# Performance work log

Hardware: AMD Instinct MI355X
Metric: run time of the kernel (lower is better)

Reference implementation:

```python
import jax, jax.numpy as jnp
import numpy as np

EPS = float(jnp.finfo(jnp.float32).eps)


def _mlp(x, W1, b1, W2, b2, W3, b3):
    h = jax.nn.relu(x @ W1 + b1)
    h = jax.nn.relu(h @ W2 + b2)
    return h @ W3 + b3


def setup_inputs() -> dict:
    B, D_A, D_B, K, H = 131072, 16, 16, 32, 256
    key = jax.random.key(0)
    ks = jax.random.split(key, 13)
    def lin(k, fi, fo):
        return jax.random.normal(k, (fi, fo), jnp.float32) * (fi ** -0.5)
    inp = {
        "x": jax.random.uniform(ks[0], (B, D_A + D_B), jnp.float32),
        "hW1": lin(ks[1], D_A, H), "hb1": jnp.zeros((H,), jnp.float32),
        "hW2": lin(ks[2], H, H),   "hb2": jnp.zeros((H,), jnp.float32),
        "hW3": lin(ks[3], H, D_B * (K + 1)), "hb3": jnp.zeros((D_B * (K + 1),), jnp.float32),
        "wW1": lin(ks[4], D_A, H), "wb1": jnp.zeros((H,), jnp.float32),
        "wW2": lin(ks[5], H, H),   "wb2": jnp.zeros((H,), jnp.float32),
        "wW3": lin(ks[6], H, D_B * K), "wb3": jnp.zeros((D_B * K,), jnp.float32),
        "A_dims": jnp.arange(0, 32, 2, dtype=jnp.int32),
        "B_dims": jnp.arange(1, 32, 2, dtype=jnp.int32),
    }
    return inp


def reference(x, hW1, hb1, hW2, hb2, hW3, hb3, wW1, wb1, wW2, wb2, wW3, wb3, A_dims, B_dims):
    B = x.shape[0]
    D_B = B_dims.shape[0]
    K = wW3.shape[1] // D_B
    x_A = x[:, A_dims]               # (B, D_A)
    x_B = x[:, B_dims]               # (B, D_B)

    raw_h = _mlp(x_A, hW1, hb1, hW2, hb2, hW3, hb3).reshape(B, D_B, K + 1)
    heights = jax.nn.softplus(raw_h) + EPS
    raw_w = _mlp(x_A, wW1, wb1, wW2, wb2, wW3, wb3).reshape(B, D_B, K)
    widths = jax.nn.softmax(raw_w, axis=-1)
    zeros = jnp.zeros((B, D_B, 1), x.dtype)
    bins = jnp.concatenate([zeros, jnp.cumsum(widths, axis=-1)], axis=-1)  # (B, D_B, K+1)

    # preprocess_params_2: normalise PDF heights and bin areas
    bin_widths = bins[:, :, 1:] - bins[:, :, :-1]
    bin_areas = 0.5 * (heights[:, :, :-1] + heights[:, :, 1:]) * bin_widths  # (B, D_B, K)
    total_area = bin_areas.sum(axis=-1, keepdims=True)
    v = heights / total_area
    bin_areas = bin_areas / total_area

    # bin search
    i = jnp.sum(x_B[..., None] >= bins, axis=-1) - 1
    i = jnp.clip(i, 0, K - 1)                                  # (B, D_B)
    iu = i[..., None]

    x_left = jnp.take_along_axis(bins, iu, axis=2)[..., 0]
    x_right = jnp.take_along_axis(bins, iu + 1, axis=2)[..., 0]
    w_b = x_right - x_left
    v_left = jnp.take_along_axis(v, iu, axis=2)[..., 0]
    v_right = jnp.take_along_axis(v, iu + 1, axis=2)[..., 0]
    w_v = v_right - v_left

    alpha = (x_B - x_left) / (w_b + EPS)
    # cumulative area up to left edge of bin i: exclusive prefix sum then gather
    c_edges = jnp.concatenate([zeros, jnp.cumsum(bin_areas, axis=-1)], axis=-1)
    c_left = jnp.take_along_axis(c_edges, iu, axis=2)[..., 0]

    y_B = c_left + 0.5 * alpha ** 2 * w_v * w_b + alpha * v_left * w_b
    y = x.at[:, B_dims].set(y_B)
    return y
```

## Files before the change

kernel.cpp:

```cpp
#include <hip/hip_runtime.h>
#include <cmath>

typedef short short8 __attribute__((ext_vector_type(8)));
typedef short short4v __attribute__((ext_vector_type(4)));
typedef float f32x16 __attribute__((ext_vector_type(16)));

#define EPSF 1.1920929e-07f

#define LDS_A2W 0
#define LDS_A2H 33792
#define LDS_A1W 67584
#define LDS_A1H 101376
#define LDS_XA  135168
#define LDS_EW  67584
#define LDS_HH  104448
#define LDS_TOTAL 141312

#define OFF1H 0
#define OFF1W 4096
#define OFF2H 8192
#define OFF2W 73728
#define OFF3H 139264
#define OFF3W 278528

__device__ __forceinline__ unsigned short f2bf(float f) {
  union { float f; unsigned u; } v; v.f = f;
  return (unsigned short)((v.u + 0x8000u) >> 16);
}
__device__ __forceinline__ float bf2f(unsigned short h) {
  union { unsigned u; float f; } v; v.u = ((unsigned)h) << 16; return v.f;
}

__global__ void pack_weights(const float* __restrict__ hW1, const float* __restrict__ wW1,
                             const float* __restrict__ hW2, const float* __restrict__ wW2,
                             const float* __restrict__ hW3, const float* __restrict__ wW3,
                             unsigned short* __restrict__ out) {
  int tile = blockIdx.x, l = threadIdx.x;
  const float* src; unsigned short* dst; int NT, N, K, base;
  if (tile < 8)        { src = hW1; dst = out + OFF1H; NT = 8;  N = 256; K = 16;  base = tile; }
  else if (tile < 16)  { src = wW1; dst = out + OFF1W; NT = 8;  N = 256; K = 16;  base = tile - 8; }
  else if (tile < 144) { src = hW2; dst = out + OFF2H; NT = 8;  N = 256; K = 256; base = tile - 16; }
  else if (tile < 272) { src = wW2; dst = out + OFF2W; NT = 8;  N = 256; K = 256; base = tile - 144; }
  else if (tile < 544) { src = hW3; dst = out + OFF3H; NT = 17; N = 528; K = 256; base = tile - 272; }
  else                 { src = wW3; dst = out + OFF3W; NT = 16; N = 512; K = 256; base = tile - 544; }
  int nt = base % NT, kt = base / NT, KTT = K / 16;
  int n = nt * 32 + (l & 31);
  int k0 = kt * 16 + (l >> 5) * 8;
  short8 v;
  #pragma unroll
  for (int e = 0; e < 8; e++) {
    float f = (n < N && (k0 + e) < K) ? src[(k0 + e) * N + n] : 0.f;
    v[e] = (short)f2bf(f);
  }
  int idx = nt * KTT + kt;
  *(short8*)(dst + (idx * 64 + l) * 8) = v;
}

struct Acc2 { f32x16 a0, a1; };

template <int KT>
__device__ __forceinline__ Acc2 gemm_tile2(const unsigned short* __restrict__ A, int apitch,
                                           const unsigned short* __restrict__ pB, int ct,
                                           float init) {
  int l = threadIdx.x & 63;
  Acc2 r;
  #pragma unroll
  for (int i = 0; i < 16; i++) { r.a0[i] = init; r.a1[i] = init; }
  const unsigned short* aptr0 = A + (l & 31) * apitch + (l >> 5) * 8;
  const unsigned short* aptr1 = aptr0 + 32 * apitch;
  const unsigned short* bptr = pB + (ct * KT * 64 + l) * 8;
  #pragma unroll
  for (int kt = 0; kt < KT; kt++) {
    short8 b = *(const short8*)(bptr + kt * 512);
    short8 a0 = *(const short8*)(aptr0 + kt * 16);
    short8 a1 = *(const short8*)(aptr1 + kt * 16);
    r.a0 = __builtin_amdgcn_mfma_f32_32x32x16_bf16(a0, b, r.a0, 0, 0, 0);
    r.a1 = __builtin_amdgcn_mfma_f32_32x32x16_bf16(a1, b, r.a1, 0, 0, 0);
  }
  return r;
}

__device__ __forceinline__ void epi_relu2(char* lds, int oOff, Acc2 a, int ct) {
  int l = threadIdx.x & 63;
  int col = ct * 32 + (l & 31);
  unsigned short* o = (unsigned short*)(lds + oOff) + col + 4 * (l >> 5) * 264;
  #pragma unroll
  for (int r = 0; r < 16; r++) {
    int row = (r & 3) + 8 * (r >> 2);
    o[row * 264] = f2bf(fmaxf(a.a0[r], 0.f));
    o[(row + 32) * 264] = f2bf(fmaxf(a.a1[r], 0.f));
  }
}

__global__ __launch_bounds__(1024, 4) void fused_kernel(
    const float* __restrict__ x,
    const float* __restrict__ hb1, const float* __restrict__ hb2, const float* __restrict__ hb3,
    const float* __restrict__ wb1, const float* __restrict__ wb2, const float* __restrict__ wb3,
    const unsigned short* __restrict__ pw,
    float* __restrict__ y) {
  extern __shared__ char lds[];
  const int t = threadIdx.x;
  const int w = t >> 6, l = t & 63;
  const int r0 = blockIdx.x * 64;

  if (t < 512) {
    int row = t >> 3, c4 = t & 7;
    float4 v = *(const float4*)(x + (r0 + row) * 32 + c4 * 4);
    y[(r0 + row) * 32 + c4 * 4] = v.x;
    y[(r0 + row) * 32 + c4 * 4 + 2] = v.z;
    unsigned short* xa = (unsigned short*)(lds + LDS_XA) + row * 16 + c4 * 2;
    xa[0] = f2bf(v.x); xa[1] = f2bf(v.z);
  }
  __syncthreads();

  const unsigned short* XA  = (const unsigned short*)(lds + LDS_XA);
  const unsigned short* A1W = (const unsigned short*)(lds + LDS_A1W);
  const unsigned short* A1H = (const unsigned short*)(lds + LDS_A1H);
  const unsigned short* A2W = (const unsigned short*)(lds + LDS_A2W);
  const unsigned short* A2H = (const unsigned short*)(lds + LDS_A2H);
  const int ct8 = w & 7;
  const int col8 = ct8 * 32 + (l & 31);

  if (w < 8) { epi_relu2(lds, LDS_A1W, gemm_tile2<1>(XA, 16, pw + OFF1W, ct8, wb1[col8]), ct8); }
  else       { epi_relu2(lds, LDS_A1H, gemm_tile2<1>(XA, 16, pw + OFF1H, ct8, hb1[col8]), ct8); }
  __syncthreads();
  if (w < 8) { epi_relu2(lds, LDS_A2W, gemm_tile2<16>(A1W, 264, pw + OFF2W, ct8, wb2[col8]), ct8); }
  else       { epi_relu2(lds, LDS_A2H, gemm_tile2<16>(A1H, 264, pw + OFF2H, ct8, hb2[col8]), ct8); }
  __syncthreads();

  #pragma unroll 1
  for (int H = 0; H < 2; H++) {
    for (int u = w; u < 17; u += 16) {
      if (u < 8) {
        int ctg = H * 8 + u;
        Acc2 a = gemm_tile2<16>(A2W, 264, pw + OFF3W, ctg, wb3[ctg * 32 + (l & 31)]);
        unsigned short* o = (unsigned short*)(lds + LDS_EW) + (ctg & 7) * 36 + (l & 31)
                            + 4 * (l >> 5) * 288;
        #pragma unroll
        for (int r = 0; r < 16; r++) {
          int row = (r & 3) + 8 * (r >> 2);
          o[row * 288] = f2bf(__expf(a.a0[r]));
          o[(row + 32) * 288] = f2bf(__expf(a.a1[r]));
        }
      } else {
        int ctg = (u - 8) + 8 * H;
        int c = ctg * 32 + (l & 31);
        float bv = (c < 528) ? hb3[c] : 0.f;
        Acc2 a = gemm_tile2<16>(A2H, 264, pw + OFF3H, ctg, bv);
        if (c >= 264 * H && c < 264 * (H + 1)) {
          unsigned d = ((unsigned)c * 993u) >> 15;
          int j = c - 33 * (int)d;
          unsigned short* o = (unsigned short*)(lds + LDS_HH) + ((int)d & 7) * 36 + j
                              + 4 * (l >> 5) * 288;
          #pragma unroll
          for (int r = 0; r < 16; r++) {
            int row = (r & 3) + 8 * (r >> 2);
            float v0 = a.a0[r];
            o[row * 288] = f2bf(fmaxf(v0, 0.f) + __logf(1.f + __expf(-fabsf(v0))) + EPSF);
            float v1 = a.a1[r];
            o[(row + 32) * 288] = f2bf(fmaxf(v1, 0.f) + __logf(1.f + __expf(-fabsf(v1))) + EPSF);
          }
        }
      }
    }
    __syncthreads();

    {
      int p = t >> 1, half = t & 1;
      int row = p >> 3, dl = p & 7, dg = H * 8 + dl;
      const unsigned short* EWb = (const unsigned short*)(lds + LDS_EW) + row * 288 + dl * 36;
      const unsigned short* HHb = (const unsigned short*)(lds + LDS_HH) + row * 288 + dl * 36;
      const unsigned short* EWp = EWb + half * 16;
      const unsigned short* HHp = HHb + half * 16;
      float e[16], hh[17];
      #pragma unroll
      for (int i = 0; i < 4; i++) {
        short4v ev = *(const short4v*)(EWp + i * 4);
        short4v hv = *(const short4v*)(HHp + i * 4);
        #pragma unroll
        for (int jj = 0; jj < 4; jj++) {
          e[i * 4 + jj] = bf2f((unsigned short)ev[jj]);
          hh[i * 4 + jj] = bf2f((unsigned short)hv[jj]);
        }
      }
      hh[16] = bf2f(HHp[16]);
      float se = 0.f;
      #pragma unroll
      for (int k = 0; k < 16; k++) se += e[k];
      float so = __shfl_xor(se, 1);
      float s = se + so;
      float xbv = x[(r0 + row) * 32 + 2 * dg + 1];
      float xbs = xbv * s;
      float bl0 = half ? so : 0.f;
      int fnd = (xbs >= bl0) ? 1 : 0;
      float bl = bl0, cl2 = 0.f, sxl = bl0, scl2 = 0.f;
      int ki = 0;
      #pragma unroll
      for (int k = 0; k < 16; k++) {
        bool c = (xbs >= bl);
        ki   = c ? k   : ki;
        sxl  = c ? bl  : sxl;
        scl2 = c ? cl2 : scl2;
        cl2 += (hh[k] + hh[k + 1]) * e[k];
        bl  += e[k];
      }
      float cl2o = __shfl_xor(cl2, 1);
      float S2 = cl2 + cl2o;
      if (half) scl2 += cl2o;
      int   o_ki   = __shfl_xor(ki, 1);
      float o_sxl  = __shfl_xor(sxl, 1);
      float o_scl2 = __shfl_xor(scl2, 1);
      int   o_fnd  = __shfl_xor(fnd, 1);
      bool other = half ? (fnd == 0) : (o_fnd != 0);
      int   gki   = other ? o_ki   : ki;
      int   ghalf = other ? (half ^ 1) : half;
      float gsxl  = other ? o_sxl  : sxl;
      float gscl2 = other ? o_scl2 : scl2;
      int go = ghalf * 16 + gki;
      float sew = bf2f(EWb[go]);
      float shl = bf2f(HHb[go]);
      float shr = bf2f(HHb[go + 1]);
      float alpha = (xbs - gsxl) / (sew + EPSF);
      float yv = (gscl2 + (alpha * alpha * (shr - shl) + 2.f * alpha * shl) * sew) / S2;
      if (!half) y[(r0 + row) * 32 + 2 * dg + 1] = yv;
    }
    __syncthreads();
  }
}

extern "C" void kernel_launch(void* const* d_in, const int* in_sizes, int n_in,
                              void* d_out, int out_size, void* d_ws, size_t ws_size,
                              hipStream_t stream) {
  const float* x   = (const float*)d_in[0];
  const float* hW1 = (const float*)d_in[1];
  const float* hb1 = (const float*)d_in[2];
  const float* hW2 = (const float*)d_in[3];
  const float* hb2 = (const float*)d_in[4];
  const float* hW3 = (const float*)d_in[5];
  const float* hb3 = (const float*)d_in[6];
  const float* wW1 = (const float*)d_in[7];
  const float* wb1 = (const float*)d_in[8];
  const float* wW2 = (const float*)d_in[9];
  const float* wb2 = (const float*)d_in[10];
  const float* wW3 = (const float*)d_in[11];
  const float* wb3 = (const float*)d_in[12];
  unsigned short* pw = (unsigned short*)d_ws;

  pack_weights<<<800, 64, 0, stream>>>(hW1, wW1, hW2, wW2, hW3, wW3, pw);

  hipFuncSetAttribute((const void*)fused_kernel,
                      hipFuncAttributeMaxDynamicSharedMemorySize, LDS_TOTAL);
  fused_kernel<<<2048, 1024, LDS_TOTAL, stream>>>(
      x, hb1, hb2, hb3, wb1, wb2, wb3, pw, (float*)d_out);
}
```

Before: 190.5 us.

## Prefetch next-layer weight fragments into registers during MFMA loops and unroll H phases

Restructures the fused MLP+spline kernel so each wave prefetches its layer-2 and layer-3 weight fragments from global memory into registers while the previous layer's MFMA loop runs, unrolls the two H phases explicitly, and preloads the x values used by the spline step. __syncthreads is replaced with an lgkmcnt wait plus s_barrier, and launch bounds drop from 4 to 1 block per CU minimum. The aim is to hide global weight-load latency behind matrix math. In exchange register pressure rises sharply (16-32 short8 fragments held live), and the new barrier only waits on LDS/scalar counters.

```diff
diff --git a/kernel.cpp b/kernel.cpp
--- a/kernel.cpp
+++ b/kernel.cpp
@@ -22,6 +22,11 @@
 #define OFF2W 73728
 #define OFF3H 139264
 #define OFF3W 278528
+
+#define LGKM_BARRIER() do { \
+  asm volatile("s_waitcnt lgkmcnt(0)" ::: "memory"); \
+  __builtin_amdgcn_s_barrier(); \
+} while (0)
 
 __device__ __forceinline__ unsigned short f2bf(float f) {
   union { float f; unsigned u; } v; v.f = f;
@@ -58,29 +63,16 @@
 
 struct Acc2 { f32x16 a0, a1; };
 
-template <int KT>
-__device__ __forceinline__ Acc2 gemm_tile2(const unsigned short* __restrict__ A, int apitch,
-                                           const unsigned short* __restrict__ pB, int ct,
-                                           float init) {
-  int l = threadIdx.x & 63;
+#define MFMA(A, B, C) __builtin_amdgcn_mfma_f32_32x32x16_bf16((A), (B), (C), 0, 0, 0)
+
+__device__ __forceinline__ Acc2 acc_init(float v) {
   Acc2 r;
   #pragma unroll
-  for (int i = 0; i < 16; i++) { r.a0[i] = init; r.a1[i] = init; }
-  const unsigned short* aptr0 = A + (l & 31) * apitch + (l >> 5) * 8;
-  const unsigned short* aptr1 = aptr0 + 32 * apitch;
-  const unsigned short* bptr = pB + (ct * KT * 64 + l) * 8;
-  #pragma unroll
-  for (int kt = 0; kt < KT; kt++) {
-    short8 b = *(const short8*)(bptr + kt * 512);
-    short8 a0 = *(const short8*)(aptr0 + kt * 16);
-    short8 a1 = *(const short8*)(aptr1 + kt * 16);
-    r.a0 = __builtin_amdgcn_mfma_f32_32x32x16_bf16(a0, b, r.a0, 0, 0, 0);
-    r.a1 = __builtin_amdgcn_mfma_f32_32x32x16_bf16(a1, b, r.a1, 0, 0, 0);
-  }
+  for (int i = 0; i < 16; i++) { r.a0[i] = v; r.a1[i] = v; }
   return r;
 }
 
-__device__ __forceinline__ void epi_relu2(char* lds, int oOff, Acc2 a, int ct) {
+__device__ __forceinline__ void epi_relu2(char* lds, int oOff, const Acc2& a, int ct) {
   int l = threadIdx.x & 63;
   int col = ct * 32 + (l & 31);
   unsigned short* o = (unsigned short*)(lds + oOff) + col + 4 * (l >> 5) * 264;
@@ -92,7 +84,97 @@
   }
 }
 
-__global__ __launch_bounds__(1024, 4) void fused_kernel(
+__device__ __forceinline__ void g3_epi(char* lds, const Acc2& a, int ctg, int H, bool wnet) {
+  int l = threadIdx.x & 63;
+  if (wnet) {
+    unsigned short* o = (unsigned short*)(lds + LDS_EW) + (ctg & 7) * 36 + (l & 31)
+                        + 4 * (l >> 5) * 288;
+    #pragma unroll
+    for (int r = 0; r < 16; r++) {
+      int row = (r & 3) + 8 * (r >> 2);
+      o[row * 288] = f2bf(__expf(a.a0[r]));
+      o[(row + 32) * 288] = f2bf(__expf(a.a1[r]));
+    }
+  } else {
+    int c = ctg * 32 + (l & 31);
+    if (c >= 264 * H && c < 264 * (H + 1)) {
+      unsigned d = ((unsigned)c * 993u) >> 15;
+      int j = c - 33 * (int)d;
+      unsigned short* o = (unsigned short*)(lds + LDS_HH) + ((int)d & 7) * 36 + j
+                          + 4 * (l >> 5) * 288;
+      #pragma unroll
+      for (int r = 0; r < 16; r++) {
+        int row = (r & 3) + 8 * (r >> 2);
+        float v0 = a.a0[r];
+        o[row * 288] = f2bf(fmaxf(v0, 0.f) + __logf(1.f + __expf(-fabsf(v0))) + EPSF);
+        float v1 = a.a1[r];
+        o[(row + 32) * 288] = f2bf(fmaxf(v1, 0.f) + __logf(1.f + __expf(-fabsf(v1))) + EPSF);
+      }
+    }
+  }
+}
+
+__device__ __forceinline__ void spline_phase(char* lds, int t, int H, float xbv,
+                                             float* __restrict__ y, int r0) {
+  int p = t >> 1, half = t & 1;
+  int row = p >> 3, dl = p & 7, dg = H * 8 + dl;
+  const unsigned short* EWb = (const unsigned short*)(lds + LDS_EW) + row * 288 + dl * 36;
+  const unsigned short* HHb = (const unsigned short*)(lds + LDS_HH) + row * 288 + dl * 36;
+  const unsigned short* EWp = EWb + half * 16;
+  const unsigned short* HHp = HHb + half * 16;
+  float e[16], hh[17];
+  #pragma unroll
+  for (int i = 0; i < 4; i++) {
+    short4v ev = *(const short4v*)(EWp + i * 4);
+    short4v hv = *(const short4v*)(HHp + i * 4);
+    #pragma unroll
+    for (int jj = 0; jj < 4; jj++) {
+      e[i * 4 + jj] = bf2f((unsigned short)ev[jj]);
+      hh[i * 4 + jj] = bf2f((unsigned short)hv[jj]);
+    }
+  }
+  hh[16] = bf2f(HHp[16]);
+  float se = 0.f;
+  #pragma unroll
+  for (int k = 0; k < 16; k++) se += e[k];
+  float so = __shfl_xor(se, 1);
+  float s = se + so;
+  float xbs = xbv * s;
+  float bl0 = half ? so : 0.f;
+  int fnd = (xbs >= bl0) ? 1 : 0;
+  float bl = bl0, cl2 = 0.f, sxl = bl0, scl2 = 0.f;
+  int ki = 0;
+  #pragma unroll
+  for (int k = 0; k < 16; k++) {
+    bool c = (xbs >= bl);
+    ki   = c ? k   : ki;
+    sxl  = c ? bl  : sxl;
+    scl2 = c ? cl2 : scl2;
+    cl2 += (hh[k] + hh[k + 1]) * e[k];
+    bl  += e[k];
+  }
+  float cl2o = __shfl_xor(cl2, 1);
+  float S2 = cl2 + cl2o;
+  if (half) scl2 += cl2o;
+  int   o_ki   = __shfl_xor(ki, 1);
+  float o_sxl  = __shfl_xor(sxl, 1);
+  float o_scl2 = __shfl_xor(scl2, 1);
+  int   o_fnd  = __shfl_xor(fnd, 1);
+  bool other = half ? (fnd == 0) : (o_fnd != 0);
+  int   gki   = other ? o_ki   : ki;
+  int   ghalf = other ? (half ^ 1) : half;
+  float gsxl  = other ? o_sxl  : sxl;
+  float gscl2 = other ? o_scl2 : scl2;
+  int go = ghalf * 16 + gki;
+  float sew = bf2f(EWb[go]);
+  float shl = bf2f(HHb[go]);
+  float shr = bf2f(HHb[go + 1]);
+  float alpha = (xbs - gsxl) / (sew + EPSF);
+  float yv = (gscl2 + (alpha * alpha * (shr - shl) + 2.f * alpha * shl) * sew) / S2;
+  if (!half) y[(r0 + row) * 32 + 2 * dg + 1] = yv;
+}
+
+__global__ __launch_bounds__(1024, 1) void fused_kernel(
     const float* __restrict__ x,
     const float* __restrict__ hb1, const float* __restrict__ hb2, const float* __restrict__ hb3,
     const float* __restrict__ wb1, const float* __restrict__ wb2, const float* __restrict__ wb3,
@@ -102,130 +184,138 @@
   const int t = threadIdx.x;
   const int w = t >> 6, l = t & 63;
   const int r0 = blockIdx.x * 64;
+  const bool wnet = (w < 8);
+  const int ct8 = w & 7;
+
+  float4 xv;
+  int xrow = t >> 3, xc4 = t & 7;
+  if (t < 512) xv = *(const float4*)(x + (r0 + xrow) * 32 + xc4 * 4);
+  int sp_p = t >> 1;
+  int sp_row = sp_p >> 3, sp_dl = sp_p & 7;
+  float xs0 = x[(r0 + sp_row) * 32 + 2 * sp_dl + 1];
+  float xs1 = x[(r0 + sp_row) * 32 + 2 * (8 + sp_dl) + 1];
+
+  const unsigned short* bL1 = pw + (wnet ? OFF1W : OFF1H) + (ct8 * 64 + l) * 8;
+  const unsigned short* bL2 = pw + (wnet ? OFF2W : OFF2H) + (ct8 * 16 * 64 + l) * 8;
+  short8 fL1 = *(const short8*)bL1;
+  short8 fL2[16];
+  #pragma unroll
+  for (int kt = 0; kt < 16; kt++) fL2[kt] = *(const short8*)(bL2 + kt * 512);
 
   if (t < 512) {
-    int row = t >> 3, c4 = t & 7;
-    float4 v = *(const float4*)(x + (r0 + row) * 32 + c4 * 4);
-    y[(r0 + row) * 32 + c4 * 4] = v.x;
-    y[(r0 + row) * 32 + c4 * 4 + 2] = v.z;
-    unsigned short* xa = (unsigned short*)(lds + LDS_XA) + row * 16 + c4 * 2;
-    xa[0] = f2bf(v.x); xa[1] = f2bf(v.z);
-  }
-  __syncthreads();
+    y[(r0 + xrow) * 32 + xc4 * 4] = xv.x;
+    y[(r0 + xrow) * 32 + xc4 * 4 + 2] = xv.z;
+    unsigned short* xa = (unsigned short*)(lds + LDS_XA) + xrow * 16 + xc4 * 2;
+    xa[0] = f2bf(xv.x); xa[1] = f2bf(xv.z);
+  }
+  LGKM_BARRIER();
 
   const unsigned short* XA  = (const unsigned short*)(lds + LDS_XA);
-  const unsigned short* A1W = (const unsigned short*)(lds + LDS_A1W);
-  const unsigned short* A1H = (const unsigned short*)(lds + LDS_A1H);
-  const unsigned short* A2W = (const unsigned short*)(lds + LDS_A2W);
-  const unsigned short* A2H = (const unsigned short*)(lds + LDS_A2H);
-  const int ct8 = w & 7;
   const int col8 = ct8 * 32 + (l & 31);
 
-  if (w < 8) { epi_relu2(lds, LDS_A1W, gemm_tile2<1>(XA, 16, pw + OFF1W, ct8, wb1[col8]), ct8); }
-  else       { epi_relu2(lds, LDS_A1H, gemm_tile2<1>(XA, 16, pw + OFF1H, ct8, hb1[col8]), ct8); }
-  __syncthreads();
-  if (w < 8) { epi_relu2(lds, LDS_A2W, gemm_tile2<16>(A1W, 264, pw + OFF2W, ct8, wb2[col8]), ct8); }
-  else       { epi_relu2(lds, LDS_A2H, gemm_tile2<16>(A1H, 264, pw + OFF2H, ct8, hb2[col8]), ct8); }
-  __syncthreads();
-
-  #pragma unroll 1
-  for (int H = 0; H < 2; H++) {
-    for (int u = w; u < 17; u += 16) {
-      if (u < 8) {
-        int ctg = H * 8 + u;
-        Acc2 a = gemm_tile2<16>(A2W, 264, pw + OFF3W, ctg, wb3[ctg * 32 + (l & 31)]);
-        unsigned short* o = (unsigned short*)(lds + LDS_EW) + (ctg & 7) * 36 + (l & 31)
-                            + 4 * (l >> 5) * 288;
-        #pragma unroll
-        for (int r = 0; r < 16; r++) {
-          int row = (r & 3) + 8 * (r >> 2);
-          o[row * 288] = f2bf(__expf(a.a0[r]));
-          o[(row + 32) * 288] = f2bf(__expf(a.a1[r]));
-        }
-      } else {
-        int ctg = (u - 8) + 8 * H;
-        int c = ctg * 32 + (l & 31);
-        float bv = (c < 528) ? hb3[c] : 0.f;
-        Acc2 a = gemm_tile2<16>(A2H, 264, pw + OFF3H, ctg, bv);
-        if (c >= 264 * H && c < 264 * (H + 1)) {
-          unsigned d = ((unsigned)c * 993u) >> 15;
-          int j = c - 33 * (int)d;
-          unsigned short* o = (unsigned short*)(lds + LDS_HH) + ((int)d & 7) * 36 + j
-                              + 4 * (l >> 5) * 288;
-          #pragma unroll
-          for (int r = 0; r < 16; r++) {
-            int row = (r & 3) + 8 * (r >> 2);
-            float v0 = a.a0[r];
-            o[row * 288] = f2bf(fmaxf(v0, 0.f) + __logf(1.f + __expf(-fabsf(v0))) + EPSF);
-            float v1 = a.a1[r];
-            o[(row + 32) * 288] = f2bf(fmaxf(v1, 0.f) + __logf(1.f + __expf(-fabsf(v1))) + EPSF);
-          }
-        }
-      }
-    }
-    __syncthreads();
-
-    {
-      int p = t >> 1, half = t & 1;
-      int row = p >> 3, dl = p & 7, dg = H * 8 + dl;
-      const unsigned short* EWb = (const unsigned short*)(lds + LDS_EW) + row * 288 + dl * 36;
-      const unsigned short* HHb = (const unsigned short*)(lds + LDS_HH) + row * 288 + dl * 36;
-      const unsigned short* EWp = EWb + half * 16;
-      const unsigned short* HHp = HHb + half * 16;
-      float e[16], hh[17];
-      #pragma unroll
-      for (int i = 0; i < 4; i++) {
-        short4v ev = *(const short4v*)(EWp + i * 4);
-        short4v hv = *(const short4v*)(HHp + i * 4);
-        #pragma unroll
-        for (int jj = 0; jj < 4; jj++) {
-          e[i * 4 + jj] = bf2f((unsigned short)ev[jj]);
-          hh[i * 4 + jj] = bf2f((unsigned short)hv[jj]);
-        }
-      }
-      hh[16] = bf2f(HHp[16]);
-      float se = 0.f;
-      #pragma unroll
-      for (int k = 0; k < 16; k++) se += e[k];
-      float so = __shfl_xor(se, 1);
-      float s = se + so;
-      float xbv = x[(r0 + row) * 32 + 2 * dg + 1];
-      float xbs = xbv * s;
-      float bl0 = half ? so : 0.f;
-      int fnd = (xbs >= bl0) ? 1 : 0;
-      float bl = bl0, cl2 = 0.f, sxl = bl0, scl2 = 0.f;
-      int ki = 0;
-      #pragma unroll
-      for (int k = 0; k < 16; k++) {
-        bool c = (xbs >= bl);
-        ki   = c ? k   : ki;
-        sxl  = c ? bl  : sxl;
-        scl2 = c ? cl2 : scl2;
-        cl2 += (hh[k] + hh[k + 1]) * e[k];
-        bl  += e[k];
-      }
-      float cl2o = __shfl_xor(cl2, 1);
-      float S2 = cl2 + cl2o;
-      if (half) scl2 += cl2o;
-      int   o_ki   = __shfl_xor(ki, 1);
-      float o_sxl  = __shfl_xor(sxl, 1);
-      float o_scl2 = __shfl_xor(scl2, 1);
-      int   o_fnd  = __shfl_xor(fnd, 1);
-      bool other = half ? (fnd == 0) : (o_fnd != 0);
-      int   gki   = other ? o_ki   : ki;
-      int   ghalf = other ? (half ^ 1) : half;
-      float gsxl  = other ? o_sxl  : sxl;
-      float gscl2 = other ? o_scl2 : scl2;
-      int go = ghalf * 16 + gki;
-      float sew = bf2f(EWb[go]);
-      float shl = bf2f(HHb[go]);
-      float shr = bf2f(HHb[go + 1]);
-      float alpha = (xbs - gsxl) / (sew + EPSF);
-      float yv = (gscl2 + (alpha * alpha * (shr - shl) + 2.f * alpha * shl) * sew) / S2;
-      if (!half) y[(r0 + row) * 32 + 2 * dg + 1] = yv;
-    }
-    __syncthreads();
-  }
+  {
+    Acc2 r = acc_init(wnet ? wb1[col8] : hb1[col8]);
+    const unsigned short* a0p = XA + (l & 31) * 16 + (l >> 5) * 8;
+    short8 a0 = *(const short8*)a0p;
+    short8 a1 = *(const short8*)(a0p + 32 * 16);
+    r.a0 = MFMA(a0, fL1, r.a0);
+    r.a1 = MFMA(a1, fL1, r.a1);
+    epi_relu2(lds, wnet ? LDS_A1W : LDS_A1H, r, ct8);
+  }
+  LGKM_BARRIER();
+
+  const int ctg0 = wnet ? w : (w - 8);
+  const int ctg1 = ctg0 + 8;
+  const unsigned short* bG3a = pw + (wnet ? OFF3W : OFF3H) + (ctg0 * 16 * 64 + l) * 8;
+  const unsigned short* bG3b = pw + (wnet ? OFF3W : OFF3H) + (ctg1 * 16 * 64 + l) * 8;
+  short8 fG3a[16];
+  {
+    Acc2 r = acc_init(wnet ? wb2[col8] : hb2[col8]);
+    const unsigned short* A1n = (const unsigned short*)(lds + (wnet ? LDS_A1W : LDS_A1H));
+    const unsigned short* a0p = A1n + (l & 31) * 264 + (l >> 5) * 8;
+    #pragma unroll
+    for (int kt = 0; kt < 16; kt++) {
+      short8 a0 = *(const short8*)(a0p + kt * 16);
+      short8 a1 = *(const short8*)(a0p + 32 * 264 + kt * 16);
+      r.a0 = MFMA(a0, fL2[kt], r.a0);
+      r.a1 = MFMA(a1, fL2[kt], r.a1);
+      fG3a[kt] = *(const short8*)(bG3a + kt * 512);
+    }
+    epi_relu2(lds, wnet ? LDS_A2W : LDS_A2H, r, ct8);
+  }
+  LGKM_BARRIER();
+
+  const unsigned short* A2n = (const unsigned short*)(lds + (wnet ? LDS_A2W : LDS_A2H));
+  const unsigned short* a2p = A2n + (l & 31) * 264 + (l >> 5) * 8;
+  const unsigned short* A2Hp = (const unsigned short*)(lds + LDS_A2H);
+  const unsigned short* a2hp = A2Hp + (l & 31) * 264 + (l >> 5) * 8;
+
+  short8 fG3b[16];
+  {
+    float binit;
+    if (wnet) binit = wb3[ctg0 * 32 + (l & 31)];
+    else { int c = ctg0 * 32 + (l & 31); binit = (c < 528) ? hb3[c] : 0.f; }
+    Acc2 a = acc_init(binit);
+    #pragma unroll
+    for (int kt = 0; kt < 16; kt++) {
+      short8 a0 = *(const short8*)(a2p + kt * 16);
+      short8 a1 = *(const short8*)(a2p + 32 * 264 + kt * 16);
+      a.a0 = MFMA(a0, fG3a[kt], a.a0);
+      a.a1 = MFMA(a1, fG3a[kt], a.a1);
+      fG3b[kt] = *(const short8*)(bG3b + kt * 512);
+    }
+    g3_epi(lds, a, ctg0, 0, wnet);
+  }
+  if (w == 0) {
+    const unsigned short* bx = pw + OFF3H + (8 * 16 * 64 + l) * 8;
+    int c = 8 * 32 + (l & 31);
+    Acc2 a = acc_init((c < 528) ? hb3[c] : 0.f);
+    #pragma unroll
+    for (int kt = 0; kt < 16; kt++) {
+      short8 a0 = *(const short8*)(a2hp + kt * 16);
+      short8 a1 = *(const short8*)(a2hp + 32 * 264 + kt * 16);
+      short8 b = *(const short8*)(bx + kt * 512);
+      a.a0 = MFMA(a0, b, a.a0);
+      a.a1 = MFMA(a1, b, a.a1);
+    }
+    g3_epi(lds, a, 8, 0, false);
+  }
+  LGKM_BARRIER();
+
+  spline_phase(lds, t, 0, xs0, y, r0);
+  LGKM_BARRIER();
+
+  {
+    float binit;
+    if (wnet) binit = wb3[ctg1 * 32 + (l & 31)];
+    else { int c = ctg1 * 32 + (l & 31); binit = (c < 528) ? hb3[c] : 0.f; }
+    Acc2 a = acc_init(binit);
+    #pragma unroll
+    for (int kt = 0; kt < 16; kt++) {
+      short8 a0 = *(const short8*)(a2p + kt * 16);
+      short8 a1 = *(const short8*)(a2p + 32 * 264 + kt * 16);
+      a.a0 = MFMA(a0, fG3b[kt], a.a0);
+      a.a1 = MFMA(a1, fG3b[kt], a.a1);
+    }
+    g3_epi(lds, a, ctg1, 1, wnet);
+  }
+  if (w == 0) {
+    const unsigned short* bx = pw + OFF3H + (16 * 16 * 64 + l) * 8;
+    int c = 16 * 32 + (l & 31);
+    Acc2 a = acc_init((c < 528) ? hb3[c] : 0.f);
+    #pragma unroll
+    for (int kt = 0; kt < 16; kt++) {
+      short8 a0 = *(const short8*)(a2hp + kt * 16);
+      short8 a1 = *(const short8*)(a2hp + 32 * 264 + kt * 16);
+      short8 b = *(const short8*)(bx + kt * 512);
+      a.a0 = MFMA(a0, b, a.a0);
+      a.a1 = MFMA(a1, b, a.a1);
+    }
+    g3_epi(lds, a, 16, 1, false);
+  }
+  LGKM_BARRIER();
+
+  spline_phase(lds, t, 1, xs1, y, r0);
 }
 
 extern "C" void kernel_launch(void* const* d_in, const int* in_sizes, int n_in,
```

New measurement: 208.3 us. 1.09x slower.
